# Kernel optimization log

Measured on AMD Instinct MI355X. Metric: run time of the kernel, lower is better.

Reference implementation:

```python
import jax, jax.numpy as jnp
import numpy as np

D_MODEL = 256
NUM_HEADS = 8
D_K = D_MODEL // NUM_HEADS
BATCH = 32
SEQ = 1024


def setup_inputs() -> dict:
    key = jax.random.key(0)
    ks = jax.random.split(key, 11)
    s = 1.0 / np.sqrt(D_MODEL)
    x = jax.random.normal(ks[0], (BATCH, SEQ, D_MODEL), dtype=jnp.float32)
    attn_mask = jax.random.randint(ks[1], (SEQ, SEQ), 0, 2) > 0  # bool topology mask
    # ensure self-attention allowed so no row is fully masked
    attn_mask = attn_mask | jnp.eye(SEQ, dtype=bool)
    Wq = jax.random.normal(ks[2], (D_MODEL, D_MODEL), jnp.float32) * s
    bq = jax.random.normal(ks[3], (D_MODEL,), jnp.float32) * s
    Wk = jax.random.normal(ks[4], (D_MODEL, D_MODEL), jnp.float32) * s
    bk = jax.random.normal(ks[5], (D_MODEL,), jnp.float32) * s
    Wv = jax.random.normal(ks[6], (D_MODEL, D_MODEL), jnp.float32) * s
    bv = jax.random.normal(ks[7], (D_MODEL,), jnp.float32) * s
    Wo = jax.random.normal(ks[8], (D_MODEL, D_MODEL), jnp.float32) * s
    bo = jax.random.normal(ks[9], (D_MODEL,), jnp.float32) * s
    return {"x": x, "attn_mask": attn_mask, "Wq": Wq, "bq": bq, "Wk": Wk,
            "bk": bk, "Wv": Wv, "bv": bv, "Wo": Wo, "bo": bo}


def reference(x, attn_mask, Wq, bq, Wk, bk, Wv, bv, Wo, bo):
    B, S, _ = x.shape
    scale = 1.0 / jnp.sqrt(jnp.asarray(D_K, x.dtype))
    def split_heads(t):  # (B,S,D) -> (B,H,S,d_k)
        return t.reshape(B, S, NUM_HEADS, D_K).transpose(0, 2, 1, 3)
    Q = split_heads(x @ Wq.T + bq)
    K = split_heads(x @ Wk.T + bk)
    V = split_heads(x @ Wv.T + bv)
    scores = jnp.einsum('bhqd,bhkd->bhqk', Q, K) * scale
    scores = jnp.where(attn_mask[None, None, :, :], scores, jnp.asarray(-1e9, scores.dtype))
    attn = jax.nn.softmax(scores, axis=-1)
    out = jnp.einsum('bhqk,bhkd->bhqd', attn, V)
    out = out.transpose(0, 2, 1, 3).reshape(B, S, D_MODEL)
    return out @ Wo.T + bo
```

## Files before the change

### kernel.cpp

```cpp
#include <hip/hip_runtime.h>
#include <hip/hip_fp16.h>
#include <stdint.h>

#define B_ 32
#define S_ 1024
#define DM 256
#define H_ 8
#define M_ (B_*S_)

typedef _Float16 f16;
typedef _Float16 f16x8 __attribute__((ext_vector_type(8)));
typedef _Float16 f16x4 __attribute__((ext_vector_type(4)));
typedef float f32x4 __attribute__((ext_vector_type(4)));

static __device__ __forceinline__ void gload16(const void* g, void* lds) {
  __builtin_amdgcn_global_load_lds(
      (const __attribute__((address_space(1))) void*)(uintptr_t)g,
      (__attribute__((address_space(3))) void*)(uintptr_t)lds, 16, 0, 0);
}

__global__ __launch_bounds__(256) void cvt_kernel(const float* __restrict__ in,
                                                  f16* __restrict__ out, int n4) {
  int i = blockIdx.x * blockDim.x + threadIdx.x;
  int stride = gridDim.x * blockDim.x;
  for (; i < n4; i += stride) {
    float4 v = reinterpret_cast<const float4*>(in)[i];
    f16x4 h = {(f16)v.x, (f16)v.y, (f16)v.z, (f16)v.w};
    reinterpret_cast<f16x4*>(out)[i] = h;
  }
}

__global__ __launch_bounds__(256) void pack_mask_kernel(const int* __restrict__ mask,
                                                        unsigned* __restrict__ pm, int nw) {
  int t = blockIdx.x * blockDim.x + threadIdx.x;
  if (t >= nw) return;
  const int* p = mask + (size_t)t * 32;
  unsigned bits = 0;
#pragma unroll
  for (int i = 0; i < 32; ++i) bits |= (p[i] != 0 ? 1u : 0u) << i;
  pm[t] = bits;
}

__global__ __launch_bounds__(256) void qkv_gemm_kernel(
    const f16* __restrict__ xh, const f16* __restrict__ wh,
    const float* __restrict__ bq, const float* __restrict__ bk, const float* __restrict__ bv,
    f16* __restrict__ qh, f16* __restrict__ kh, f16* __restrict__ vth) {
  __shared__ __align__(16) f16 Al[128 * 32];
  __shared__ __align__(16) f16 Bl[128 * 32];
  const int tid = threadIdx.x;
  const int w = tid >> 6, l = tid & 63;
  const int mt = blockIdx.x / 6, nt = blockIdx.x % 6;
  const int mbase = mt * 128, nbase = nt * 128;
  const int wm = w >> 1, wn = w & 1;
  const int lg = l >> 4, lr = l & 15;
  f32x4 acc[4][4] = {};
  for (int ks = 0; ks < 8; ++ks) {
    __syncthreads();
#pragma unroll
    for (int j = 0; j < 2; ++j) {
      int c = (j * 4 + w) * 64 + l;
      gload16(xh + (size_t)(mbase + (c >> 2)) * 256 + ks * 32 + (c & 3) * 8,
              (char*)Al + (j * 4 + w) * 1024);
      gload16(wh + (size_t)(nbase + (c >> 2)) * 256 + ks * 32 + (c & 3) * 8,
              (char*)Bl + (j * 4 + w) * 1024);
    }
    __syncthreads();
    f16x8 af[4], bf[4];
#pragma unroll
    for (int i = 0; i < 4; ++i)
      af[i] = *(const f16x8*)((const char*)Al + (wm * 64 + i * 16 + lr) * 64 + lg * 16);
#pragma unroll
    for (int i = 0; i < 4; ++i)
      bf[i] = *(const f16x8*)((const char*)Bl + (wn * 64 + i * 16 + lr) * 64 + lg * 16);
#pragma unroll
    for (int mi = 0; mi < 4; ++mi)
#pragma unroll
      for (int ni = 0; ni < 4; ++ni)
        acc[mi][ni] = __builtin_amdgcn_mfma_f32_16x16x32_f16(af[mi], bf[ni], acc[mi][ni], 0, 0, 0);
  }
  const int proj = nt >> 1;
  const float* bias = proj == 0 ? bq : (proj == 1 ? bk : bv);
#pragma unroll
  for (int mi = 0; mi < 4; ++mi) {
#pragma unroll
    for (int ni = 0; ni < 4; ++ni) {
      int n = nbase + wn * 64 + ni * 16 + lr;
      float bb = bias[n & 255];
#pragma unroll
      for (int r = 0; r < 4; ++r) {
        int m = mbase + wm * 64 + mi * 16 + lg * 4 + r;
        f16 hv = (f16)(acc[mi][ni][r] + bb);
        int b = m >> 10, s = m & 1023;
        int hh = (n >> 5) & 7, d = n & 31;
        int bh = b * 8 + hh;
        if (proj == 0)      qh[((size_t)bh * 1024 + s) * 32 + d] = hv;
        else if (proj == 1) kh[((size_t)bh * 1024 + s) * 32 + d] = hv;
        else                vth[((size_t)bh * 32 + d) * 1024 + s] = hv;
      }
    }
  }
}

__global__ __launch_bounds__(256) void attn_kernel(
    const f16* __restrict__ qh, const f16* __restrict__ kh, const f16* __restrict__ vth,
    const unsigned* __restrict__ pm, f16* __restrict__ attnh) {
  __shared__ __align__(16) f16 Kl[64 * 32];
  __shared__ __align__(16) f16 Vtl[32 * 64];
  __shared__ __align__(16) f16 Pl[4][16 * 64];
  const int tid = threadIdx.x;
  const int w = tid >> 6, l = tid & 63;
  const int bh = blockIdx.x >> 4, qt = blockIdx.x & 15;
  const int qbase = qt * 64;
  const int lg = l >> 4, lr = l & 15;
  const float scale = 0.17677669529663687f;

  f16x8 qf = *(const f16x8*)(qh + ((size_t)bh * 1024 + qbase + w * 16 + lr) * 32 + lg * 8);
  float mrun[4], lrun[4];
#pragma unroll
  for (int r = 0; r < 4; ++r) { mrun[r] = -__builtin_inff(); lrun[r] = 0.f; }
  f32x4 oacc[2] = {};
  const f32x4 zero = {};

  for (int t = 0; t < 16; ++t) {
    const int kvb = t * 64;
    __syncthreads();
    {
      int c = w * 64 + l;
      gload16(kh + ((size_t)bh * 1024 + kvb + (c >> 2)) * 32 + (c & 3) * 8,
              (char*)Kl + w * 1024);
      int cd = c ^ ((c >> 3) & 7);
      gload16(vth + ((size_t)bh * 32 + (c >> 3)) * 1024 + kvb + (cd & 7) * 8,
              (char*)Vtl + w * 1024);
    }
    __syncthreads();

    f32x4 sc[4];
#pragma unroll
    for (int kt = 0; kt < 4; ++kt) {
      f16x8 kf = *(const f16x8*)((const char*)Kl + (kt * 16 + lr) * 64 + lg * 16);
      sc[kt] = __builtin_amdgcn_mfma_f32_16x16x32_f16(qf, kf, zero, 0, 0, 0);
    }
#pragma unroll
    for (int r = 0; r < 4; ++r) {
      int qg = qbase + w * 16 + lg * 4 + r;
#pragma unroll
      for (int wi = 0; wi < 2; ++wi) {
        unsigned word = pm[qg * 32 + t * 2 + wi];
#pragma unroll
        for (int k2 = 0; k2 < 2; ++k2) {
          int kt = wi * 2 + k2;
          float v = sc[kt][r] * scale;
          unsigned bit = (word >> (k2 * 16 + lr)) & 1u;
          sc[kt][r] = bit ? v : -1e9f;
        }
      }
    }
    float pr[4][4];
#pragma unroll
    for (int r = 0; r < 4; ++r) {
      float rm = fmaxf(fmaxf(sc[0][r], sc[1][r]), fmaxf(sc[2][r], sc[3][r]));
#pragma unroll
      for (int off = 8; off >= 1; off >>= 1) rm = fmaxf(rm, __shfl_xor(rm, off));
      float mnew = fmaxf(mrun[r], rm);
      float alpha = __expf(mrun[r] - mnew);
      mrun[r] = mnew;
      float rs = 0.f;
#pragma unroll
      for (int kt = 0; kt < 4; ++kt) {
        float p = __expf(sc[kt][r] - mnew);
        pr[kt][r] = p;
        rs += p;
      }
#pragma unroll
      for (int off = 8; off >= 1; off >>= 1) rs += __shfl_xor(rs, off);
      lrun[r] = lrun[r] * alpha + rs;
      oacc[0][r] *= alpha;
      oacc[1][r] *= alpha;
    }
#pragma unroll
    for (int kt = 0; kt < 4; ++kt) {
      int col = kt * 16 + lr;
      int cc = col >> 3;
#pragma unroll
      for (int r = 0; r < 4; ++r) {
        int row = lg * 4 + r;
        *((f16*)((char*)Pl[w] + row * 128 + ((cc ^ (row & 7)) << 4) + (col & 7) * 2)) =
            (f16)pr[kt][r];
      }
    }
#pragma unroll
    for (int ss = 0; ss < 2; ++ss) {
      f16x8 pa = *(const f16x8*)((const char*)Pl[w] + lr * 128 + (((ss * 4 + lg) ^ (lr & 7)) << 4));
#pragma unroll
      for (int dt = 0; dt < 2; ++dt) {
        int vrow = dt * 16 + lr;
        f16x8 vf = *(const f16x8*)((const char*)Vtl + vrow * 128 + (((ss * 4 + lg) ^ (vrow & 7)) << 4));
        oacc[dt] = __builtin_amdgcn_mfma_f32_16x16x32_f16(pa, vf, oacc[dt], 0, 0, 0);
      }
    }
  }
  const int b = bh >> 3, hh = bh & 7;
#pragma unroll
  for (int r = 0; r < 4; ++r) {
    float inv = 1.f / lrun[r];
    int q = qbase + w * 16 + lg * 4 + r;
    size_t rowoff = ((size_t)b * 1024 + q) * 256 + hh * 32;
    attnh[rowoff + lr]      = (f16)(oacc[0][r] * inv);
    attnh[rowoff + 16 + lr] = (f16)(oacc[1][r] * inv);
  }
}

__global__ __launch_bounds__(256) void out_gemm_kernel(
    const f16* __restrict__ ah, const f16* __restrict__ wh,
    const float* __restrict__ bo, float* __restrict__ out) {
  __shared__ __align__(16) f16 Al[128 * 32];
  __shared__ __align__(16) f16 Bl[128 * 32];
  const int tid = threadIdx.x;
  const int w = tid >> 6, l = tid & 63;
  const int mt = blockIdx.x >> 1, nt = blockIdx.x & 1;
  const int mbase = mt * 128, nbase = nt * 128;
  const int wm = w >> 1, wn = w & 1;
  const int lg = l >> 4, lr = l & 15;
  f32x4 acc[4][4] = {};
  for (int ks = 0; ks < 8; ++ks) {
    __syncthreads();
#pragma unroll
    for (int j = 0; j < 2; ++j) {
      int c = (j * 4 + w) * 64 + l;
      gload16(ah + (size_t)(mbase + (c >> 2)) * 256 + ks * 32 + (c & 3) * 8,
              (char*)Al + (j * 4 + w) * 1024);
      gload16(wh + (size_t)(nbase + (c >> 2)) * 256 + ks * 32 + (c & 3) * 8,
              (char*)Bl + (j * 4 + w) * 1024);
    }
    __syncthreads();
    f16x8 af[4], bf[4];
#pragma unroll
    for (int i = 0; i < 4; ++i)
      af[i] = *(const f16x8*)((const char*)Al + (wm * 64 + i * 16 + lr) * 64 + lg * 16);
#pragma unroll
    for (int i = 0; i < 4; ++i)
      bf[i] = *(const f16x8*)((const char*)Bl + (wn * 64 + i * 16 + lr) * 64 + lg * 16);
#pragma unroll
    for (int mi = 0; mi < 4; ++mi)
#pragma unroll
      for (int ni = 0; ni < 4; ++ni)
        acc[mi][ni] = __builtin_amdgcn_mfma_f32_16x16x32_f16(af[mi], bf[ni], acc[mi][ni], 0, 0, 0);
  }
#pragma unroll
  for (int mi = 0; mi < 4; ++mi) {
#pragma unroll
    for (int ni = 0; ni < 4; ++ni) {
      int n = nbase + wn * 64 + ni * 16 + lr;
      float bb = bo[n];
#pragma unroll
      for (int r = 0; r < 4; ++r) {
        int m = mbase + wm * 64 + mi * 16 + lg * 4 + r;
        out[(size_t)m * 256 + n] = acc[mi][ni][r] + bb;
      }
    }
  }
}

extern "C" void kernel_launch(void* const* d_in, const int* in_sizes, int n_in,
                              void* d_out, int out_size, void* d_ws, size_t ws_size,
                              hipStream_t stream) {
  const float* x  = (const float*)d_in[0];
  const int* mask = (const int*)d_in[1];
  const float* Wq = (const float*)d_in[2];
  const float* bq = (const float*)d_in[3];
  const float* Wk = (const float*)d_in[4];
  const float* bk = (const float*)d_in[5];
  const float* Wv = (const float*)d_in[6];
  const float* bv = (const float*)d_in[7];
  const float* Wo = (const float*)d_in[8];
  const float* bo = (const float*)d_in[9];
  float* out = (float*)d_out;
  char* ws = (char*)d_ws;

  f16* xh    = (f16*)(ws);
  f16* attnh = (f16*)(ws);
  f16* qh    = (f16*)(ws + 16777216);
  f16* kh    = (f16*)(ws + 33554432);
  f16* vth   = (f16*)(ws + 50331648);
  f16* wqkvh = (f16*)(ws + 67108864);
  f16* woh   = (f16*)(ws + 67502080);
  unsigned* pm = (unsigned*)(ws + 67633152);

  cvt_kernel<<<2048, 256, 0, stream>>>(x, xh, (B_*S_*DM) / 4);
  cvt_kernel<<<64, 256, 0, stream>>>(Wq, wqkvh, 16384);
  cvt_kernel<<<64, 256, 0, stream>>>(Wk, wqkvh + 65536, 16384);
  cvt_kernel<<<64, 256, 0, stream>>>(Wv, wqkvh + 131072, 16384);
  cvt_kernel<<<64, 256, 0, stream>>>(Wo, woh, 16384);
  pack_mask_kernel<<<128, 256, 0, stream>>>(mask, pm, 32768);
  qkv_gemm_kernel<<<1536, 256, 0, stream>>>(xh, wqkvh, bq, bk, bv, qh, kh, vth);
  attn_kernel<<<4096, 256, 0, stream>>>(qh, kh, vth, pm, attnh);
  out_gemm_kernel<<<512, 256, 0, stream>>>(attnh, woh, bo, out);
}
```

Measured before the change: 347.5 us.

## Double-buffer attention K/V tiles, fold scale into Q, use exp2 with lazy rescale

Rewrites the attention inner loop: K/V tiles are double-buffered and prefetched with global-to-LDS loads, so loading overlaps compute. The softmax scale and log2(e) are folded into Q at the projection, letting the loop use raw v_exp_f32, and the running max is rescaled only when it grows by more than 8. The mask is expanded to fp16 0/1 pairs and multiplied into the probabilities, and row sums come from an MFMA against a ones vector. This removes per-element mask bit extraction, shuffles and divides, but the expanded mask is 16x larger and fully masked tiles now contribute zero rather than -1e9.

```diff
diff --git a/kernel.cpp b/kernel.cpp
--- a/kernel.cpp
+++ b/kernel.cpp
@@ -6,7 +6,6 @@
 #define S_ 1024
 #define DM 256
 #define H_ 8
-#define M_ (B_*S_)
 
 typedef _Float16 f16;
 typedef _Float16 f16x8 __attribute__((ext_vector_type(8)));
@@ -17,6 +16,15 @@
   __builtin_amdgcn_global_load_lds(
       (const __attribute__((address_space(1))) void*)(uintptr_t)g,
       (__attribute__((address_space(3))) void*)(uintptr_t)lds, 16, 0, 0);
+}
+static __device__ __forceinline__ float ex2(float x) {
+  float r; asm("v_exp_f32 %0, %1" : "=v"(r) : "v"(x)); return r;
+}
+static __device__ __forceinline__ unsigned pkrtz(float a, float b) {
+  unsigned r; asm("v_cvt_pkrtz_f16_f32 %0, %1, %2" : "=v"(r) : "v"(a), "v"(b)); return r;
+}
+static __device__ __forceinline__ unsigned pkmul(unsigned a, unsigned b) {
+  unsigned r; asm("v_pk_mul_f16 %0, %1, %2" : "=v"(r) : "v"(a), "v"(b)); return r;
 }
 
 __global__ __launch_bounds__(256) void cvt_kernel(const float* __restrict__ in,
@@ -30,15 +38,12 @@
   }
 }
 
-__global__ __launch_bounds__(256) void pack_mask_kernel(const int* __restrict__ mask,
-                                                        unsigned* __restrict__ pm, int nw) {
+__global__ __launch_bounds__(256) void expand_mask_kernel(const int* __restrict__ mask,
+                                                          unsigned* __restrict__ pmx, int n) {
   int t = blockIdx.x * blockDim.x + threadIdx.x;
-  if (t >= nw) return;
-  const int* p = mask + (size_t)t * 32;
-  unsigned bits = 0;
-#pragma unroll
-  for (int i = 0; i < 32; ++i) bits |= (p[i] != 0 ? 1u : 0u) << i;
-  pm[t] = bits;
+  if (t >= n) return;
+  int2 mm = reinterpret_cast<const int2*>(mask)[t];
+  pmx[t] = (mm.x ? 0x3C00u : 0u) | (mm.y ? 0x3C000000u : 0u);
 }
 
 __global__ __launch_bounds__(256) void qkv_gemm_kernel(
@@ -80,6 +85,7 @@
   }
   const int proj = nt >> 1;
   const float* bias = proj == 0 ? bq : (proj == 1 ? bk : bv);
+  const float qsc = 0.25504182524668425f;
 #pragma unroll
   for (int mi = 0; mi < 4; ++mi) {
 #pragma unroll
@@ -89,7 +95,9 @@
 #pragma unroll
       for (int r = 0; r < 4; ++r) {
         int m = mbase + wm * 64 + mi * 16 + lg * 4 + r;
-        f16 hv = (f16)(acc[mi][ni][r] + bb);
+        float val = acc[mi][ni][r] + bb;
+        if (proj == 0) val *= qsc;
+        f16 hv = (f16)val;
         int b = m >> 10, s = m & 1023;
         int hh = (n >> 5) & 7, d = n & 31;
         int bh = b * 8 + hh;
@@ -103,108 +111,114 @@
 
 __global__ __launch_bounds__(256) void attn_kernel(
     const f16* __restrict__ qh, const f16* __restrict__ kh, const f16* __restrict__ vth,
-    const unsigned* __restrict__ pm, f16* __restrict__ attnh) {
-  __shared__ __align__(16) f16 Kl[64 * 32];
-  __shared__ __align__(16) f16 Vtl[32 * 64];
+    const unsigned* __restrict__ pmx, f16* __restrict__ attnh) {
+  __shared__ __align__(16) f16 Kl[2][64 * 32];
+  __shared__ __align__(16) f16 Vtl[2][32 * 64];
   __shared__ __align__(16) f16 Pl[4][16 * 64];
   const int tid = threadIdx.x;
   const int w = tid >> 6, l = tid & 63;
   const int bh = blockIdx.x >> 4, qt = blockIdx.x & 15;
   const int qbase = qt * 64;
   const int lg = l >> 4, lr = l & 15;
-  const float scale = 0.17677669529663687f;
-
-  f16x8 qf = *(const f16x8*)(qh + ((size_t)bh * 1024 + qbase + w * 16 + lr) * 32 + lg * 8);
-  float mrun[4], lrun[4];
-#pragma unroll
-  for (int r = 0; r < 4; ++r) { mrun[r] = -__builtin_inff(); lrun[r] = 0.f; }
+  const int q = qbase + w * 16 + lr;
+
+  f16x8 qf = *(const f16x8*)(qh + ((size_t)bh * 1024 + q) * 32 + lg * 8);
+  const unsigned* mrow = pmx + (size_t)q * 512;
+
+  float mrun = -1e30f;
   f32x4 oacc[2] = {};
+  f32x4 lacc = {};
   const f32x4 zero = {};
+  f16x8 ones;
+#pragma unroll
+  for (int i = 0; i < 8; ++i) ones[i] = (f16)1.0f;
+
+  const f16* kgbase = kh + ((size_t)bh * 1024 + (tid >> 2)) * 32 + (tid & 3) * 8;
+  const f16* vgbase = vth + ((size_t)bh * 32 + (tid >> 3)) * 1024 + ((tid & 7) ^ ((tid >> 3) & 7)) * 8;
+
+  uint2 mc[4], mn[4];
+#pragma unroll
+  for (int k = 0; k < 4; ++k) mc[k] = *(const uint2*)(mrow + 0 * 32 + k * 8 + lg * 2);
+  gload16(kgbase, (char*)Kl[0] + tid * 16);
+  gload16(vgbase, (char*)Vtl[0] + tid * 16);
 
   for (int t = 0; t < 16; ++t) {
-    const int kvb = t * 64;
-    __syncthreads();
-    {
-      int c = w * 64 + l;
-      gload16(kh + ((size_t)bh * 1024 + kvb + (c >> 2)) * 32 + (c & 3) * 8,
-              (char*)Kl + w * 1024);
-      int cd = c ^ ((c >> 3) & 7);
-      gload16(vth + ((size_t)bh * 32 + (c >> 3)) * 1024 + kvb + (cd & 7) * 8,
-              (char*)Vtl + w * 1024);
-    }
-    __syncthreads();
+    asm volatile("" ::: "memory");
+    __builtin_amdgcn_s_barrier();
+    const int nxt = t + 1;
+    if (nxt < 16) {
+#pragma unroll
+      for (int k = 0; k < 4; ++k) mn[k] = *(const uint2*)(mrow + nxt * 32 + k * 8 + lg * 2);
+      const int nb = nxt & 1;
+      gload16(kgbase + (size_t)nxt * 64 * 32, (char*)Kl[nb] + tid * 16);
+      gload16(vgbase + (size_t)nxt * 64, (char*)Vtl[nb] + tid * 16);
+      asm volatile("s_waitcnt vmcnt(6)" ::: "memory");
+    } else {
+      asm volatile("s_waitcnt vmcnt(0)" ::: "memory");
+    }
+    __builtin_amdgcn_s_barrier();
+
+    const char* kbuf = (const char*)Kl[t & 1];
+    const char* vbuf = (const char*)Vtl[t & 1];
 
     f32x4 sc[4];
 #pragma unroll
     for (int kt = 0; kt < 4; ++kt) {
-      f16x8 kf = *(const f16x8*)((const char*)Kl + (kt * 16 + lr) * 64 + lg * 16);
-      sc[kt] = __builtin_amdgcn_mfma_f32_16x16x32_f16(qf, kf, zero, 0, 0, 0);
-    }
-#pragma unroll
-    for (int r = 0; r < 4; ++r) {
-      int qg = qbase + w * 16 + lg * 4 + r;
-#pragma unroll
-      for (int wi = 0; wi < 2; ++wi) {
-        unsigned word = pm[qg * 32 + t * 2 + wi];
-#pragma unroll
-        for (int k2 = 0; k2 < 2; ++k2) {
-          int kt = wi * 2 + k2;
-          float v = sc[kt][r] * scale;
-          unsigned bit = (word >> (k2 * 16 + lr)) & 1u;
-          sc[kt][r] = bit ? v : -1e9f;
-        }
+      f16x8 kf = *(const f16x8*)(kbuf + (kt * 16 + lr) * 64 + lg * 16);
+      sc[kt] = __builtin_amdgcn_mfma_f32_16x16x32_f16(kf, qf, zero, 0, 0, 0);
+    }
+    float t0 = fmaxf(fmaxf(sc[0][0], sc[0][1]), fmaxf(sc[0][2], sc[0][3]));
+    float t1 = fmaxf(fmaxf(sc[1][0], sc[1][1]), fmaxf(sc[1][2], sc[1][3]));
+    float t2 = fmaxf(fmaxf(sc[2][0], sc[2][1]), fmaxf(sc[2][2], sc[2][3]));
+    float t3 = fmaxf(fmaxf(sc[3][0], sc[3][1]), fmaxf(sc[3][2], sc[3][3]));
+    float pmax = fmaxf(fmaxf(t0, t1), fmaxf(t2, t3));
+    pmax = fmaxf(pmax, __shfl_xor(pmax, 16));
+    pmax = fmaxf(pmax, __shfl_xor(pmax, 32));
+    if (__any(pmax > mrun + 8.0f)) {
+      float mnew = fmaxf(mrun, pmax);
+      float alpha = ex2(mrun - mnew);
+      mrun = mnew;
+#pragma unroll
+      for (int r = 0; r < 4; ++r) {
+        float ar = __shfl(alpha, (l & 48) | (lg * 4 + r), 64);
+        oacc[0][r] *= ar;
+        oacc[1][r] *= ar;
+        lacc[r] *= ar;
       }
     }
-    float pr[4][4];
-#pragma unroll
-    for (int r = 0; r < 4; ++r) {
-      float rm = fmaxf(fmaxf(sc[0][r], sc[1][r]), fmaxf(sc[2][r], sc[3][r]));
-#pragma unroll
-      for (int off = 8; off >= 1; off >>= 1) rm = fmaxf(rm, __shfl_xor(rm, off));
-      float mnew = fmaxf(mrun[r], rm);
-      float alpha = __expf(mrun[r] - mnew);
-      mrun[r] = mnew;
-      float rs = 0.f;
-#pragma unroll
-      for (int kt = 0; kt < 4; ++kt) {
-        float p = __expf(sc[kt][r] - mnew);
-        pr[kt][r] = p;
-        rs += p;
-      }
-#pragma unroll
-      for (int off = 8; off >= 1; off >>= 1) rs += __shfl_xor(rs, off);
-      lrun[r] = lrun[r] * alpha + rs;
-      oacc[0][r] *= alpha;
-      oacc[1][r] *= alpha;
-    }
+    char* pbuf = (char*)Pl[w];
 #pragma unroll
     for (int kt = 0; kt < 4; ++kt) {
-      int col = kt * 16 + lr;
-      int cc = col >> 3;
-#pragma unroll
-      for (int r = 0; r < 4; ++r) {
-        int row = lg * 4 + r;
-        *((f16*)((char*)Pl[w] + row * 128 + ((cc ^ (row & 7)) << 4) + (col & 7) * 2)) =
-            (f16)pr[kt][r];
-      }
+      float p0 = ex2(sc[kt][0] - mrun);
+      float p1 = ex2(sc[kt][1] - mrun);
+      float p2 = ex2(sc[kt][2] - mrun);
+      float p3 = ex2(sc[kt][3] - mrun);
+      unsigned lo = pkmul(pkrtz(p0, p1), mc[kt].x);
+      unsigned hi = pkmul(pkrtz(p2, p3), mc[kt].y);
+      *(uint64_t*)(pbuf + lr * 128 + ((kt * 32 + lg * 8) ^ ((lr & 7) << 4))) =
+          (uint64_t)lo | ((uint64_t)hi << 32);
     }
 #pragma unroll
     for (int ss = 0; ss < 2; ++ss) {
-      f16x8 pa = *(const f16x8*)((const char*)Pl[w] + lr * 128 + (((ss * 4 + lg) ^ (lr & 7)) << 4));
+      f16x8 pa = *(const f16x8*)(pbuf + lr * 128 + ((ss * 64 + lg * 16) ^ ((lr & 7) << 4)));
+      lacc = __builtin_amdgcn_mfma_f32_16x16x32_f16(pa, ones, lacc, 0, 0, 0);
 #pragma unroll
       for (int dt = 0; dt < 2; ++dt) {
-        int vrow = dt * 16 + lr;
-        f16x8 vf = *(const f16x8*)((const char*)Vtl + vrow * 128 + (((ss * 4 + lg) ^ (vrow & 7)) << 4));
+        int vr = dt * 16 + lr;
+        f16x8 vf = *(const f16x8*)(vbuf + vr * 128 + ((ss * 64 + lg * 16) ^ ((lr & 7) << 4)));
         oacc[dt] = __builtin_amdgcn_mfma_f32_16x16x32_f16(pa, vf, oacc[dt], 0, 0, 0);
       }
     }
-  }
+#pragma unroll
+    for (int k = 0; k < 4; ++k) mc[k] = mn[k];
+  }
+
   const int b = bh >> 3, hh = bh & 7;
 #pragma unroll
   for (int r = 0; r < 4; ++r) {
-    float inv = 1.f / lrun[r];
-    int q = qbase + w * 16 + lg * 4 + r;
-    size_t rowoff = ((size_t)b * 1024 + q) * 256 + hh * 32;
+    float inv = 1.0f / lacc[r];
+    int qrow = qbase + w * 16 + lg * 4 + r;
+    size_t rowoff = ((size_t)b * 1024 + qrow) * 256 + hh * 32;
     attnh[rowoff + lr]      = (f16)(oacc[0][r] * inv);
     attnh[rowoff + 16 + lr] = (f16)(oacc[1][r] * inv);
   }
@@ -284,15 +298,15 @@
   f16* vth   = (f16*)(ws + 50331648);
   f16* wqkvh = (f16*)(ws + 67108864);
   f16* woh   = (f16*)(ws + 67502080);
-  unsigned* pm = (unsigned*)(ws + 67633152);
+  unsigned* pmx = (unsigned*)(ws + 67633152);
 
   cvt_kernel<<<2048, 256, 0, stream>>>(x, xh, (B_*S_*DM) / 4);
   cvt_kernel<<<64, 256, 0, stream>>>(Wq, wqkvh, 16384);
   cvt_kernel<<<64, 256, 0, stream>>>(Wk, wqkvh + 65536, 16384);
   cvt_kernel<<<64, 256, 0, stream>>>(Wv, wqkvh + 131072, 16384);
   cvt_kernel<<<64, 256, 0, stream>>>(Wo, woh, 16384);
-  pack_mask_kernel<<<128, 256, 0, stream>>>(mask, pm, 32768);
+  expand_mask_kernel<<<2048, 256, 0, stream>>>(mask, pmx, 1024 * 512);
   qkv_gemm_kernel<<<1536, 256, 0, stream>>>(xh, wqkvh, bq, bk, bv, qh, kh, vth);
-  attn_kernel<<<4096, 256, 0, stream>>>(qh, kh, vth, pm, attnh);
+  attn_kernel<<<4096, 256, 0, stream>>>(qh, kh, vth, pmx, attnh);
   out_gemm_kernel<<<512, 256, 0, stream>>>(attnh, woh, bo, out);
 }
```

After: 309.3 us. 1.12x faster.
